# Performance work log

Measured on AMD Instinct MI355X. Metric: run time of the kernel, lower is better.

The kernel has to match this reference:

```python
import jax, jax.numpy as jnp
import numpy as np

B, N, D = 4, 160, 64
ZI, ZE, L, LE = 64, 64, 4, 8
H1, H2 = 128, 64


def setup_inputs() -> dict:
    key = jax.random.key(0)
    ks = jax.random.split(key, 20)
    s = 0.05
    inp = {
        "node_embeddings": jax.random.normal(ks[0], (B, N, D), jnp.float32),
        "z_intra_t": jax.random.normal(ks[1], (B, ZI), jnp.float32),
        "z_inter_t": jax.random.normal(ks[2], (B, ZE), jnp.float32),
        # lag embedding table
        "lag_emb": jax.random.normal(ks[3], (L, LE), jnp.float32),
        # instantaneous reasoner: (2D+ZI)->128->64->1
        "Wi1": jax.random.normal(ks[4], (2 * D + ZI, H1), jnp.float32) * s,
        "bi1": jnp.zeros((H1,), jnp.float32),
        "Wi2": jax.random.normal(ks[5], (H1, H2), jnp.float32) * s,
        "bi2": jnp.zeros((H2,), jnp.float32),
        "Wi3": jax.random.normal(ks[6], (H2, 1), jnp.float32) * s,
        "bi3": jnp.zeros((1,), jnp.float32),
        # lagged reasoner: (2D+ZE+LE)->128->64->1
        "Wl1": jax.random.normal(ks[7], (2 * D + ZE + LE, H1), jnp.float32) * s,
        "bl1": jnp.zeros((H1,), jnp.float32),
        "Wl2": jax.random.normal(ks[8], (H1, H2), jnp.float32) * s,
        "bl2": jnp.zeros((H2,), jnp.float32),
        "Wl3": jax.random.normal(ks[9], (H2, 1), jnp.float32) * s,
        "bl3": jnp.zeros((1,), jnp.float32),
    }
    return inp


def reference(node_embeddings, z_intra_t, z_inter_t, lag_emb,
              Wi1, bi1, Wi2, bi2, Wi3, bi3,
              Wl1, bl1, Wl2, bl2, Wl3, bl3):
    # Instead of materializing concat([h_i, h_j, z, ...]) over N*N pairs,
    # split the first linear layer's weight along its input rows; the sum of
    # per-part projections equals the linear over the concatenation.
    ne = node_embeddings  # [B, N, D]

    # --- instantaneous reasoner ---
    Wi1_a, Wi1_b, Wi1_z = Wi1[:D], Wi1[D:2 * D], Wi1[2 * D:]
    pi = ne @ Wi1_a          # [B, N, H1] projection of h_i
    pj = ne @ Wi1_b          # [B, N, H1] projection of h_j
    pz = z_intra_t @ Wi1_z   # [B, H1]
    h = jax.nn.relu(pi[:, :, None, :] + pj[:, None, :, :]
                    + pz[:, None, None, :] + bi1)          # [B, N, N, H1]
    h = jax.nn.relu(h @ Wi2 + bi2)                         # [B, N, N, H2]
    W_logits = (h @ Wi3 + bi3)[..., 0]                     # [B, N, N]

    # --- lagged reasoner ---
    Wl1_a, Wl1_b = Wl1[:D], Wl1[D:2 * D]
    Wl1_z, Wl1_l = Wl1[2 * D:2 * D + ZE], Wl1[2 * D + ZE:]
    qi = ne @ Wl1_a          # [B, N, H1]
    qj = ne @ Wl1_b          # [B, N, H1]
    qz = z_inter_t @ Wl1_z   # [B, H1]
    ql = lag_emb @ Wl1_l     # [L, H1]
    g = jax.nn.relu(qi[:, None, :, None, :] + qj[:, None, None, :, :]
                    + qz[:, None, None, None, :] + ql[None, :, None, None, :]
                    + bl1)                                 # [B, L, N, N, H1]
    g = jax.nn.relu(g @ Wl2 + bl2)                         # [B, L, N, N, H2]
    A_logits = (g @ Wl3 + bl3)[..., 0]                     # [B, L, N, N]

    mask = 1.0 - jnp.eye(N, dtype=ne.dtype)
    W_t = jax.nn.sigmoid(W_logits) * mask
    A_lags_t = jax.nn.sigmoid(A_logits) * mask
    return (W_t, A_lags_t)
```

## Files before the change

kernel.cpp:

```cpp
#include <hip/hip_runtime.h>
#include <hip/hip_bf16.h>

#define B_   4
#define N_   160
#define D_   64
#define ZI_  64
#define H1_  128
#define H2_  64
#define L_   4
#define LE_  8

typedef __bf16 bf16x8 __attribute__((ext_vector_type(8)));
typedef float  f32x4  __attribute__((ext_vector_type(4)));
typedef unsigned int u32x4 __attribute__((ext_vector_type(4)));

static __device__ __forceinline__ unsigned pk_bf16(float a, float b) {
    __hip_bfloat162 h = __float22bfloat162_rn(float2{a, b});
    union { __hip_bfloat162 h; unsigned u; } c;
    c.h = h;
    return c.u;
}

__global__ __launch_bounds__(128) void stage_a(
    const float* __restrict__ ne,
    const float* __restrict__ zi,
    const float* __restrict__ ze,
    const float* __restrict__ lag,
    const float* __restrict__ Wi1,
    const float* __restrict__ bi1,
    const float* __restrict__ Wl1,
    const float* __restrict__ bl1,
    const float* __restrict__ Wi2,
    const float* __restrict__ bi2,
    const float* __restrict__ Wi3,
    const float* __restrict__ bi3,
    const float* __restrict__ Wl2,
    const float* __restrict__ bl2,
    const float* __restrict__ Wl3,
    const float* __restrict__ bl3,
    float* __restrict__ ui, float* __restrict__ uq,
    __bf16* __restrict__ vpi, __bf16* __restrict__ vpl,
    char* __restrict__ blob_i, char* __restrict__ blob_l)
{
    const int bi = blockIdx.x;
    const int b  = bi / N_;
    const int h  = threadIdx.x;

    const float* nerow = ne + bi * D_;

    float pi_ = 0.f, pj_ = 0.f, qi_ = 0.f, qj_ = 0.f;
#pragma unroll 16
    for (int d = 0; d < D_; ++d) {
        const float a = nerow[d];
        pi_ += a * Wi1[d * H1_ + h];
        pj_ += a * Wi1[(D_ + d) * H1_ + h];
        qi_ += a * Wl1[d * H1_ + h];
        qj_ += a * Wl1[(D_ + d) * H1_ + h];
    }
    float pz = 0.f, qz = 0.f;
#pragma unroll 16
    for (int z = 0; z < ZI_; ++z) {
        pz += zi[b * ZI_ + z] * Wi1[(2 * D_ + z) * H1_ + h];
        qz += ze[b * ZI_ + z] * Wl1[(2 * D_ + z) * H1_ + h];
    }

    const int r7 = h & 7;
    const int hp = (h & ~7) | ((r7 & 1) ? (4 + (r7 >> 1)) : (r7 >> 1));

    ui[bi * H1_ + hp] = pi_ + pz + bi1[h];

    const int hsw = (((h >> 3) ^ (bi & 7)) << 3) | (h & 7);
    vpi[bi * H1_ + hsw] = (__bf16)pj_;
    vpl[bi * H1_ + hsw] = (__bf16)qj_;

    const float qbase = qi_ + qz + bl1[h];
#pragma unroll
    for (int l = 0; l < L_; ++l) {
        float ql = 0.f;
#pragma unroll
        for (int e = 0; e < LE_; ++e)
            ql += lag[l * LE_ + e] * Wl1[(2 * D_ + ZI_ + e) * H1_ + h];
        uq[((b * L_ + l) * N_ + (bi % N_)) * H1_ + hp] = qbase + ql;
    }

    if (bi < 2) {
        const float* Wsrc = (bi == 0) ? Wi2 : Wl2;
        char* blob = (bi == 0) ? blob_i : blob_l;
        __bf16* Wdst = (__bf16*)blob;
#pragma unroll
        for (int r = 0; r < 8; ++r) {
            const int fc = h + 128 * r;
            const int kt = fc >> 8, ct = (fc >> 6) & 3;
            const int q = (fc >> 4) & 3, c = fc & 15;
            bf16x8 t;
#pragma unroll
            for (int j = 0; j < 8; ++j)
                t[j] = (__bf16)Wsrc[(32 * kt + 8 * q + j) * H2_ + 16 * ct + c];
            *(bf16x8*)(Wdst + fc * 8) = t;
        }
        float* bdst = (float*)(blob + 16384);
        const float* b2s = (bi == 0) ? bi2 : bl2;
        const float* w3s = (bi == 0) ? Wi3 : Wl3;
        const float* b3s = (bi == 0) ? bi3 : bl3;
        if (h < H2_) bdst[h] = b2s[h];
        if (h < H2_) bdst[128 + h] = w3s[h];
        if (h == 0)  bdst[256] = b3s[0];
    }
}

__global__ __launch_bounds__(512, 6) void stage_b(
    const float* __restrict__ ui, const float* __restrict__ uq,
    const __bf16* __restrict__ vpi, const __bf16* __restrict__ vpl,
    const char* __restrict__ blob_i, const char* __restrict__ blob_l,
    float* __restrict__ out)
{
    __shared__ __align__(16) char lds[45056];
    __bf16* panel = (__bf16*)lds;
    char*   blob  = lds + 20480;
    float*  ulds  = (float*)(lds + 40960);

    const int t    = threadIdx.x;
    const int wid  = t >> 6;
    const int lane = t & 63;
    const int q = lane >> 4;
    const int c = lane & 15;

    const int blk    = blockIdx.x;
    const int rowgrp = blk >> 1;
    const int half   = blk & 1;
    const int wave   = rowgrp * 8 + wid;
    const int row0   = rowgrp * 8;

    const __bf16* psrc;
    const char*   bsrc;
    const float*  usrc;
    if (rowgrp < 80) {
        psrc = vpi + (rowgrp / 20) * (N_ * H1_);
        bsrc = blob_i;
        usrc = ui + row0 * H1_;
    } else {
        psrc = vpl + ((rowgrp - 80) / 80) * (N_ * H1_);
        bsrc = blob_l;
        usrc = uq + (row0 - B_ * N_) * H1_;
    }
    psrc += 80 * half * H1_;

    for (int g = wid; g < 44; g += 8) {
        const char* src;
        if (g < 20)      src = (const char*)psrc + (g << 10);
        else if (g < 40) src = bsrc + ((g - 20) << 10);
        else             src = (const char*)usrc + ((g - 40) << 10);
        __builtin_amdgcn_global_load_lds(
            (const __attribute__((address_space(1))) void*)(src + lane * 16),
            (__attribute__((address_space(3))) void*)(lds + (g << 10)),
            16, 0, 0);
    }

    long obase;
    int  i;
    if (wave < B_ * N_) {
        i = wave % N_;
        obase = (long)wave * N_;
    } else {
        const int w2i = wave - B_ * N_;
        i = w2i % N_;
        obase = (long)B_ * N_ * N_ + (long)w2i * N_;
    }

    __syncthreads();

    const float* bf32 = (const float*)(blob + 16384);
    float b2c[4], w3c[4];
#pragma unroll
    for (int ct = 0; ct < 4; ++ct) {
        b2c[ct] = bf32[16 * ct + c];
        w3c[ct] = bf32[128 + 16 * ct + c];
    }
    const float b3f = bf32[256];

    const float* ubase = ulds + wid * H1_;

    for (int jt = 0; jt < 5; ++jt) {
        asm volatile("" ::: "memory");
        const __bf16* prow = panel + (16 * jt + c) * H1_;
        f32x4 acc[4];
#pragma unroll
        for (int ct = 0; ct < 4; ++ct)
            acc[ct] = (f32x4){b2c[ct], b2c[ct], b2c[ct], b2c[ct]};

#pragma unroll
        for (int kt = 0; kt < 4; ++kt) {
            const u32x4 vw = *(const u32x4*)(prow + (((4 * kt + q) ^ (c & 7)) << 3));
            const f32x4 ue = *(const f32x4*)(ubase + 32 * kt + 8 * q);
            const f32x4 uo = *(const f32x4*)(ubase + 32 * kt + 8 * q + 4);
            union { bf16x8 v; unsigned d[4]; } a;
#pragma unroll
            for (int d = 0; d < 4; ++d) {
                const unsigned w = vw[d];
                const float lo = __uint_as_float(w << 16) + ue[d];
                const float hi = __uint_as_float(w & 0xffff0000u) + uo[d];
                a.d[d] = pk_bf16(fmaxf(lo, 0.f), fmaxf(hi, 0.f));
            }
#pragma unroll
            for (int ct = 0; ct < 4; ++ct) {
                const bf16x8 bfrag =
                    *(const bf16x8*)(blob + ((kt * 4 + ct) * 64 + lane) * 16);
                acc[ct] = __builtin_amdgcn_mfma_f32_16x16x32_bf16(
                    a.v, bfrag, acc[ct], 0, 0, 0);
            }
        }

        float logit[4];
#pragma unroll
        for (int r = 0; r < 4; ++r) {
            float p = 0.f;
#pragma unroll
            for (int ct = 0; ct < 4; ++ct)
                p += fmaxf(acc[ct][r], 0.f) * w3c[ct];
            p += __shfl_xor(p, 1);
            p += __shfl_xor(p, 2);
            p += __shfl_xor(p, 4);
            p += __shfl_xor(p, 8);
            logit[r] = p;
        }

        if (c < 4) {
            const int j = 80 * half + 16 * jt + 4 * q + c;
            const float lg = logit[c] + b3f;
            const float s = (j == i) ? 0.f : 1.f / (1.f + __expf(-lg));
            out[obase + j] = s;
        }
    }
}

extern "C" void kernel_launch(void* const* d_in, const int* in_sizes, int n_in,
                              void* d_out, int out_size, void* d_ws, size_t ws_size,
                              hipStream_t stream) {
    const float* ne  = (const float*)d_in[0];
    const float* zi  = (const float*)d_in[1];
    const float* ze  = (const float*)d_in[2];
    const float* lag = (const float*)d_in[3];
    const float* Wi1 = (const float*)d_in[4];
    const float* bi1 = (const float*)d_in[5];
    const float* Wi2 = (const float*)d_in[6];
    const float* bi2 = (const float*)d_in[7];
    const float* Wi3 = (const float*)d_in[8];
    const float* bi3 = (const float*)d_in[9];
    const float* Wl1 = (const float*)d_in[10];
    const float* bl1 = (const float*)d_in[11];
    const float* Wl2 = (const float*)d_in[12];
    const float* bl2 = (const float*)d_in[13];
    const float* Wl3 = (const float*)d_in[14];
    const float* bl3 = (const float*)d_in[15];

    float*  ws     = (float*)d_ws;
    float*  ui     = ws;
    float*  uqw    = ws + 81920;
    __bf16* vpi    = (__bf16*)(ws + 409600);
    __bf16* vpl    = vpi + 81920;
    char*   blob_i = (char*)d_ws + 1966080;
    char*   blob_l = blob_i + 20480;

    stage_a<<<B_ * N_, 128, 0, stream>>>(ne, zi, ze, lag, Wi1, bi1, Wl1, bl1,
                                         Wi2, bi2, Wi3, bi3, Wl2, bl2, Wl3, bl3,
                                         ui, uqw, vpi, vpl, blob_i, blob_l);

    stage_b<<<800, 512, 0, stream>>>(
        ui, uqw, vpi, vpl, blob_i, blob_l,
        (float*)d_out);
}
```

Measured before the change: 113.2 us.

## Restructure stage_b: 4 waves per block, full j panel, weights in registers

```diff
diff --git a/kernel.cpp b/kernel.cpp
--- a/kernel.cpp
+++ b/kernel.cpp
@@ -108,16 +108,13 @@
     }
 }
 
-__global__ __launch_bounds__(512, 6) void stage_b(
+__global__ __launch_bounds__(256, 3) void stage_b(
     const float* __restrict__ ui, const float* __restrict__ uq,
     const __bf16* __restrict__ vpi, const __bf16* __restrict__ vpl,
     const char* __restrict__ blob_i, const char* __restrict__ blob_l,
     float* __restrict__ out)
 {
-    __shared__ __align__(16) char lds[45056];
-    __bf16* panel = (__bf16*)lds;
-    char*   blob  = lds + 20480;
-    float*  ulds  = (float*)(lds + 40960);
+    __shared__ __align__(16) char lds[43008];
 
     const int t    = threadIdx.x;
     const int wid  = t >> 6;
@@ -125,51 +122,40 @@
     const int q = lane >> 4;
     const int c = lane & 15;
 
-    const int blk    = blockIdx.x;
-    const int rowgrp = blk >> 1;
-    const int half   = blk & 1;
-    const int wave   = rowgrp * 8 + wid;
-    const int row0   = rowgrp * 8;
+    const int blk  = blockIdx.x;
+    const int row0 = blk * 4;
+    const int wave = row0 + wid;
 
     const __bf16* psrc;
     const char*   bsrc;
     const float*  usrc;
-    if (rowgrp < 80) {
-        psrc = vpi + (rowgrp / 20) * (N_ * H1_);
+    if (blk < 160) {
+        psrc = vpi + (blk / 40) * (N_ * H1_);
         bsrc = blob_i;
         usrc = ui + row0 * H1_;
     } else {
-        psrc = vpl + ((rowgrp - 80) / 80) * (N_ * H1_);
+        psrc = vpl + ((blk - 160) / 160) * (N_ * H1_);
         bsrc = blob_l;
         usrc = uq + (row0 - B_ * N_) * H1_;
     }
-    psrc += 80 * half * H1_;
-
-    for (int g = wid; g < 44; g += 8) {
-        const char* src;
-        if (g < 20)      src = (const char*)psrc + (g << 10);
-        else if (g < 40) src = bsrc + ((g - 20) << 10);
-        else             src = (const char*)usrc + ((g - 40) << 10);
+
+    for (int g = wid; g < 42; g += 4) {
+        const char* src = (g < 40) ? (const char*)psrc + (g << 10)
+                                   : (const char*)usrc + ((g - 40) << 10);
         __builtin_amdgcn_global_load_lds(
             (const __attribute__((address_space(1))) void*)(src + lane * 16),
             (__attribute__((address_space(3))) void*)(lds + (g << 10)),
             16, 0, 0);
     }
 
-    long obase;
-    int  i;
-    if (wave < B_ * N_) {
-        i = wave % N_;
-        obase = (long)wave * N_;
-    } else {
-        const int w2i = wave - B_ * N_;
-        i = w2i % N_;
-        obase = (long)B_ * N_ * N_ + (long)w2i * N_;
-    }
-
-    __syncthreads();
-
-    const float* bf32 = (const float*)(blob + 16384);
+    bf16x8 bfr[4][4];
+#pragma unroll
+    for (int kt = 0; kt < 4; ++kt)
+#pragma unroll
+        for (int ct = 0; ct < 4; ++ct)
+            bfr[kt][ct] = *(const bf16x8*)(bsrc + ((kt * 4 + ct) * 64 + lane) * 16);
+
+    const float* bf32 = (const float*)(bsrc + 16384);
     float b2c[4], w3c[4];
 #pragma unroll
     for (int ct = 0; ct < 4; ++ct) {
@@ -178,10 +164,22 @@
     }
     const float b3f = bf32[256];
 
-    const float* ubase = ulds + wid * H1_;
-
-    for (int jt = 0; jt < 5; ++jt) {
-        asm volatile("" ::: "memory");
+    const int  i     = (wave < B_ * N_ ? wave : wave - B_ * N_) % N_;
+    const long obase = (long)wave * N_;
+
+    __syncthreads();
+
+    const float* ubase = (const float*)(lds + 40960) + wid * H1_;
+    f32x4 ue[4], uo[4];
+#pragma unroll
+    for (int kt = 0; kt < 4; ++kt) {
+        ue[kt] = *(const f32x4*)(ubase + 32 * kt + 8 * q);
+        uo[kt] = *(const f32x4*)(ubase + 32 * kt + 8 * q + 4);
+    }
+
+    const __bf16* panel = (const __bf16*)lds;
+
+    for (int jt = 0; jt < 10; ++jt) {
         const __bf16* prow = panel + (16 * jt + c) * H1_;
         f32x4 acc[4];
 #pragma unroll
@@ -191,23 +189,18 @@
 #pragma unroll
         for (int kt = 0; kt < 4; ++kt) {
             const u32x4 vw = *(const u32x4*)(prow + (((4 * kt + q) ^ (c & 7)) << 3));
-            const f32x4 ue = *(const f32x4*)(ubase + 32 * kt + 8 * q);
-            const f32x4 uo = *(const f32x4*)(ubase + 32 * kt + 8 * q + 4);
             union { bf16x8 v; unsigned d[4]; } a;
 #pragma unroll
             for (int d = 0; d < 4; ++d) {
                 const unsigned w = vw[d];
-                const float lo = __uint_as_float(w << 16) + ue[d];
-                const float hi = __uint_as_float(w & 0xffff0000u) + uo[d];
+                const float lo = __uint_as_float(w << 16) + ue[kt][d];
+                const float hi = __uint_as_float(w & 0xffff0000u) + uo[kt][d];
                 a.d[d] = pk_bf16(fmaxf(lo, 0.f), fmaxf(hi, 0.f));
             }
 #pragma unroll
-            for (int ct = 0; ct < 4; ++ct) {
-                const bf16x8 bfrag =
-                    *(const bf16x8*)(blob + ((kt * 4 + ct) * 64 + lane) * 16);
+            for (int ct = 0; ct < 4; ++ct)
                 acc[ct] = __builtin_amdgcn_mfma_f32_16x16x32_bf16(
-                    a.v, bfrag, acc[ct], 0, 0, 0);
-            }
+                    a.v, bfr[kt][ct], acc[ct], 0, 0, 0);
         }
 
         float logit[4];
@@ -225,7 +218,7 @@
         }
 
         if (c < 4) {
-            const int j = 80 * half + 16 * jt + 4 * q + c;
+            const int j = 16 * jt + 4 * q + c;
             const float lg = logit[c] + b3f;
             const float s = (j == i) ? 0.f : 1.f / (1.f + __expf(-lg));
             out[obase + j] = s;
@@ -265,7 +258,7 @@
                                          Wi2, bi2, Wi3, bi3, Wl2, bl2, Wl3, bl3,
                                          ui, uqw, vpi, vpl, blob_i, blob_l);
 
-    stage_b<<<800, 512, 0, stream>>>(
+    stage_b<<<800, 256, 0, stream>>>(
         ui, uqw, vpi, vpl, blob_i, blob_l,
         (float*)d_out);
 }
```

Result: no change. 114.8 us (+1.4%).
